# Performance work log

Hardware: AMD Instinct MI355X
Metric: run time of the kernel (lower is better)

Reference implementation:

```python
import jax, jax.numpy as jnp
import numpy as np

NEG_BIG = -1e9

def setup_inputs() -> dict:
    key = jax.random.key(0)
    kq, kk, kv, kwq, kwk, kwv, km = jax.random.split(key, 7)
    B, S, d = 16, 1024, 512
    Q = jax.random.normal(kq, (B, S, d), dtype=jnp.float32)
    K = jax.random.normal(kk, (B, S, d), dtype=jnp.float32)
    V = jax.random.normal(kv, (B, S, d), dtype=jnp.float32)
    # nn.Linear weights [d, d]; torch applies x @ W.T
    WQ = jax.random.normal(kwq, (d, d), dtype=jnp.float32) / np.sqrt(d)
    WK = jax.random.normal(kwk, (d, d), dtype=jnp.float32) / np.sqrt(d)
    WV = jax.random.normal(kwv, (d, d), dtype=jnp.float32) / np.sqrt(d)
    mask = jax.random.randint(km, (B, S), 0, 2, dtype=jnp.int32)
    return {"Q": Q, "K": K, "V": V, "WQ": WQ, "WK": WK, "WV": WV, "mask": mask}


def reference(Q, K, V, WQ, WK, WV, mask):
    d = Q.shape[-1]
    q = jnp.einsum('bsd,ed->bse', Q, WQ)
    k = jnp.einsum('bsd,ed->bse', K, WK)
    v = jnp.einsum('bsd,ed->bse', V, WV)
    scores = jnp.einsum('bqd,bkd->bqk', q, k) / jnp.sqrt(jnp.float32(d))
    attn = jax.nn.softmax(scores, axis=-1)
    # Faithful to original: mask applied AFTER softmax with -1e9 fill
    m = mask[:, None, :]  # [B,1,S] broadcast over query dim
    attn = jnp.where(m == 0, jnp.float32(NEG_BIG), attn)
    out = jnp.einsum('bqk,bkd->bqd', attn, v)
    return (out, attn)
```

## Files before the change

### kernel.cpp

```cpp
#include <hip/hip_runtime.h>
#include <hip/hip_bf16.h>

typedef float f32x4 __attribute__((ext_vector_type(4)));
typedef __bf16 bf16x8 __attribute__((ext_vector_type(8)));
typedef unsigned short u16x8 __attribute__((ext_vector_type(8)));
typedef int i32x4 __attribute__((ext_vector_type(4)));

#define NEG_BIG_F (-1000000000.0f)
#define SCALE_F 0.044194173824159216f

__device__ __forceinline__ unsigned short f2bf(float f) {
  unsigned int u = __float_as_uint(f);
  u += 0x7FFFu + ((u >> 16) & 1u);
  return (unsigned short)(u >> 16);
}

__device__ __forceinline__ float bf2f(unsigned short h) {
  return __uint_as_float((unsigned int)h << 16);
}

__device__ __forceinline__ u16x8 cvt8(f32x4 a, f32x4 b) {
  u16x8 r;
  r[0] = f2bf(a[0]); r[1] = f2bf(a[1]); r[2] = f2bf(a[2]); r[3] = f2bf(a[3]);
  r[4] = f2bf(b[0]); r[5] = f2bf(b[1]); r[6] = f2bf(b[2]); r[7] = f2bf(b[3]);
  return r;
}

__device__ __forceinline__ void gload16(const void* g, char* l) {
  __builtin_amdgcn_global_load_lds(
      (const __attribute__((address_space(1))) unsigned int*)g,
      (__attribute__((address_space(3))) unsigned int*)l, 16, 0, 0);
}

__global__ __launch_bounds__(256) void cvtW(
    const float* __restrict__ w0, const float* __restrict__ w1,
    const float* __restrict__ w2, unsigned short* __restrict__ out)
{
  const float* src = blockIdx.z == 0 ? w0 : (blockIdx.z == 1 ? w1 : w2);
  unsigned short* dst = out + (size_t)blockIdx.z * 262144;
  const int i = (blockIdx.x * 256 + threadIdx.x) * 8;
  f32x4 a = *(const f32x4*)(src + i);
  f32x4 b = *(const f32x4*)(src + i + 4);
  *(u16x8*)&dst[i] = cvt8(a, b);
}

__global__ __launch_bounds__(512, 2) void projqk(
    const float* __restrict__ Q, const float* __restrict__ Kx,
    const unsigned short* __restrict__ wb,
    unsigned short* __restrict__ qb, unsigned short* __restrict__ kb)
{
  __shared__ __align__(16) unsigned short As[2][256][32];
  __shared__ __align__(16) unsigned short Bs[2][256][32];

  const int tid = threadIdx.x, z = blockIdx.z;
  const float* X = z ? Kx : Q;
  const unsigned short* W = wb + (size_t)z * 262144;
  unsigned short* Y = z ? kb : qb;
  const int m0 = blockIdx.x * 256, n0 = blockIdx.y * 256;
  const int lane = tid & 63, wave = tid >> 6;
  const int wr = (wave >> 2) * 128, wc = (wave & 3) * 64;
  const int fr = lane & 15, fq = lane >> 4;

  f32x4 acc[8][4] = {};

  int arow_s[2], aswz_s[2];
  const float* gAs[2];
  #pragma unroll
  for (int i = 0; i < 2; i++) {
    const int c = tid + 512 * i;
    arow_s[i] = c >> 2;
    aswz_s[i] = ((c & 3) ^ ((arow_s[i] >> 1) & 3)) * 8;
    gAs[i] = X + (size_t)(m0 + arow_s[i]) * 512 + (c & 3) * 8;
  }
  const unsigned short* gB[2]; char* lB[2];
  #pragma unroll
  for (int i = 0; i < 2; i++) {
    const int c = tid + 512 * i, row = c >> 2, slot = c & 3;
    gB[i] = W + (size_t)(n0 + row) * 512 + (slot ^ ((row >> 1) & 3)) * 8;
    lB[i] = (char*)&Bs[0][0][0] + c * 16;
  }

  f32x4 pa[2][2];
  #pragma unroll
  for (int i = 0; i < 2; i++) {
    pa[i][0] = *(const f32x4*)(gAs[i]);
    pa[i][1] = *(const f32x4*)(gAs[i] + 4);
  }
  #pragma unroll
  for (int i = 0; i < 2; i++) gload16(gB[i], lB[i]);
  #pragma unroll
  for (int i = 0; i < 2; i++)
    *(u16x8*)&As[0][arow_s[i]][aswz_s[i]] = cvt8(pa[i][0], pa[i][1]);

  int cur = 0;
  for (int kt = 0; kt < 512; kt += 32) {
    const int nb = cur ^ 1;
    if (kt < 480) {
      #pragma unroll
      for (int i = 0; i < 2; i++) {
        pa[i][0] = *(const f32x4*)(gAs[i] + kt + 32);
        pa[i][1] = *(const f32x4*)(gAs[i] + kt + 36);
      }
      #pragma unroll
      for (int i = 0; i < 2; i++) gload16(gB[i] + kt + 32, lB[i] + nb * 16384);
      asm volatile("s_waitcnt vmcnt(6) lgkmcnt(0)" ::: "memory");
    } else {
      asm volatile("s_waitcnt vmcnt(0) lgkmcnt(0)" ::: "memory");
    }
    __builtin_amdgcn_sched_barrier(0);
    __builtin_amdgcn_s_barrier();

    bf16x8 bv[4];
    #pragma unroll
    for (int nf = 0; nf < 4; nf++) {
      const int br = wc + nf * 16 + fr;
      bv[nf] = *(const bf16x8*)&Bs[cur][br][(fq ^ ((br >> 1) & 3)) * 8];
    }
    #pragma unroll
    for (int mf = 0; mf < 8; mf++) {
      const int ar = wr + mf * 16 + fr;
      bf16x8 av = *(const bf16x8*)&As[cur][ar][(fq ^ ((ar >> 1) & 3)) * 8];
      #pragma unroll
      for (int nf = 0; nf < 4; nf++)
        acc[mf][nf] = __builtin_amdgcn_mfma_f32_16x16x32_bf16(av, bv[nf], acc[mf][nf], 0, 0, 0);
    }

    if (kt < 480) {
      #pragma unroll
      for (int i = 0; i < 2; i++)
        *(u16x8*)&As[nb][arow_s[i]][aswz_s[i]] = cvt8(pa[i][0], pa[i][1]);
    }
    __builtin_amdgcn_s_barrier();
    cur = nb;
  }

  #pragma unroll
  for (int mf = 0; mf < 8; mf++)
    #pragma unroll
    for (int nf = 0; nf < 4; nf++)
      #pragma unroll
      for (int rr = 0; rr < 4; rr++) {
        const int m = m0 + wr + mf * 16 + fq * 4 + rr;
        const int n = n0 + wc + nf * 16 + fr;
        Y[(size_t)m * 512 + n] = f2bf(acc[mf][nf][rr]);
      }
}

__global__ __launch_bounds__(512, 2) void projv(
    const float* __restrict__ V, const unsigned short* __restrict__ wv,
    unsigned short* __restrict__ vt)
{
  __shared__ __align__(16) unsigned short As[2][128][32];
  __shared__ __align__(16) unsigned short Bs[2][256][32];

  const int tid = threadIdx.x;
  const int m0 = blockIdx.x * 128, n0 = blockIdx.y * 256, b = blockIdx.z;
  const int lane = tid & 63, wave = tid >> 6;
  const int wr = (wave >> 2) * 64, wc = (wave & 3) * 64;
  const int fr = lane & 15, fq = lane >> 4;

  f32x4 acc[4][4] = {};

  const int ar_s = tid >> 2, aslot = tid & 3;
  const unsigned short* gA = wv + (size_t)(m0 + ar_s) * 512 + (aslot ^ ((ar_s >> 1) & 3)) * 8;
  char* lA = (char*)&As[0][0][0] + tid * 16;

  int brow_s[2], bswz_s[2];
  const float* gBs[2];
  #pragma unroll
  for (int i = 0; i < 2; i++) {
    const int c = tid + 512 * i;
    brow_s[i] = c >> 2;
    bswz_s[i] = ((c & 3) ^ ((brow_s[i] >> 1) & 3)) * 8;
    gBs[i] = V + ((size_t)b * 1024 + n0 + brow_s[i]) * 512 + (c & 3) * 8;
  }

  f32x4 pb[2][2];
  #pragma unroll
  for (int i = 0; i < 2; i++) {
    pb[i][0] = *(const f32x4*)(gBs[i]);
    pb[i][1] = *(const f32x4*)(gBs[i] + 4);
  }
  gload16(gA, lA);
  #pragma unroll
  for (int i = 0; i < 2; i++)
    *(u16x8*)&Bs[0][brow_s[i]][bswz_s[i]] = cvt8(pb[i][0], pb[i][1]);

  int cur = 0;
  for (int kt = 0; kt < 512; kt += 32) {
    const int nb = cur ^ 1;
    if (kt < 480) {
      #pragma unroll
      for (int i = 0; i < 2; i++) {
        pb[i][0] = *(const f32x4*)(gBs[i] + kt + 32);
        pb[i][1] = *(const f32x4*)(gBs[i] + kt + 36);
      }
      gload16(gA + kt + 32, lA + nb * 8192);
      asm volatile("s_waitcnt vmcnt(5) lgkmcnt(0)" ::: "memory");
    } else {
      asm volatile("s_waitcnt vmcnt(0) lgkmcnt(0)" ::: "memory");
    }
    __builtin_amdgcn_sched_barrier(0);
    __builtin_amdgcn_s_barrier();

    bf16x8 av[4], bv[4];
    #pragma unroll
    for (int mf = 0; mf < 4; mf++) {
      const int ar = wr + mf * 16 + fr;
      av[mf] = *(const bf16x8*)&As[cur][ar][(fq ^ ((ar >> 1) & 3)) * 8];
    }
    #pragma unroll
    for (int nf = 0; nf < 4; nf++) {
      const int br = wc + nf * 16 + fr;
      bv[nf] = *(const bf16x8*)&Bs[cur][br][(fq ^ ((br >> 1) & 3)) * 8];
    }
    #pragma unroll
    for (int mf = 0; mf < 4; mf++)
      #pragma unroll
      for (int nf = 0; nf < 4; nf++)
        acc[mf][nf] = __builtin_amdgcn_mfma_f32_16x16x32_bf16(av[mf], bv[nf], acc[mf][nf], 0, 0, 0);

    if (kt < 480) {
      #pragma unroll
      for (int i = 0; i < 2; i++)
        *(u16x8*)&Bs[nb][brow_s[i]][bswz_s[i]] = cvt8(pb[i][0], pb[i][1]);
    }
    __builtin_amdgcn_s_barrier();
    cur = nb;
  }

  #pragma unroll
  for (int mf = 0; mf < 4; mf++)
    #pragma unroll
    for (int nf = 0; nf < 4; nf++)
      #pragma unroll
      for (int rr = 0; rr < 4; rr++) {
        const int e = m0 + wr + mf * 16 + fq * 4 + rr;
        const int s = n0 + wc + nf * 16 + fr;
        vt[((size_t)b * 512 + e) * 1024 + s] = f2bf(acc[mf][nf][rr]);
      }
}

__global__ __launch_bounds__(512, 2) void score256(
    const unsigned short* __restrict__ qb, const unsigned short* __restrict__ kb,
    const int* __restrict__ mask,
    unsigned short* __restrict__ P, float* __restrict__ partial)
{
  __shared__ __align__(16) unsigned short As[2][256][32];
  __shared__ __align__(16) unsigned short Bs[2][256][32];

  const int tid = threadIdx.x, bz = blockIdx.z;
  const int m0 = blockIdx.x * 256, n0 = blockIdx.y * 256;
  const int lane = tid & 63, wave = tid >> 6;
  const int wr = (wave >> 2) * 128, wc = (wave & 3) * 64;
  const int fr = lane & 15, fq = lane >> 4;

  f32x4 acc[8][4] = {};

  const unsigned short* gA[2]; char* lA[2];
  const unsigned short* gB[2]; char* lB[2];
  #pragma unroll
  for (int i = 0; i < 2; i++) {
    const int c = tid + 512 * i, row = c >> 2, slot = c & 3;
    const int sw = (slot ^ ((row >> 1) & 3)) * 8;
    gA[i] = qb + ((size_t)bz * 1024 + m0 + row) * 512 + sw;
    gB[i] = kb + ((size_t)bz * 1024 + n0 + row) * 512 + sw;
    lA[i] = (char*)&As[0][0][0] + c * 16;
    lB[i] = (char*)&Bs[0][0][0] + c * 16;
  }

  #pragma unroll
  for (int i = 0; i < 2; i++) { gload16(gA[i], lA[i]); gload16(gB[i], lB[i]); }

  int cur = 0;
  for (int kt = 0; kt < 512; kt += 32) {
    const int nb = cur ^ 1;
    if (kt < 480) {
      #pragma unroll
      for (int i = 0; i < 2; i++) {
        gload16(gA[i] + kt + 32, lA[i] + nb * 16384);
        gload16(gB[i] + kt + 32, lB[i] + nb * 16384);
      }
      asm volatile("s_waitcnt vmcnt(4) lgkmcnt(0)" ::: "memory");
    } else {
      asm volatile("s_waitcnt vmcnt(0) lgkmcnt(0)" ::: "memory");
    }
    __builtin_amdgcn_sched_barrier(0);
    __builtin_amdgcn_s_barrier();

    bf16x8 bv[4];
    #pragma unroll
    for (int nf = 0; nf < 4; nf++) {
      const int br = wc + nf * 16 + fr;
      bv[nf] = *(const bf16x8*)&Bs[cur][br][(fq ^ ((br >> 1) & 3)) * 8];
    }
    #pragma unroll
    for (int mf = 0; mf < 8; mf++) {
      const int ar = wr + mf * 16 + fr;
      bf16x8 av = *(const bf16x8*)&As[cur][ar][(fq ^ ((ar >> 1) & 3)) * 8];
      #pragma unroll
      for (int nf = 0; nf < 4; nf++)
        acc[mf][nf] = __builtin_amdgcn_mfma_f32_16x16x32_bf16(av, bv[nf], acc[mf][nf], 0, 0, 0);
    }
    __builtin_amdgcn_s_barrier();
    cur = nb;
  }

  int mcol[4];
  #pragma unroll
  for (int nf = 0; nf < 4; nf++)
    mcol[nf] = mask[bz * 1024 + n0 + wc + nf * 16 + fr];

  unsigned short* Pb = P + ((size_t)bz << 20);
  const int slot = blockIdx.y * 4 + (wave & 3);
  #pragma unroll
  for (int mf = 0; mf < 8; mf++) {
    #pragma unroll
    for (int rr = 0; rr < 4; rr++) {
      const int m = m0 + wr + mf * 16 + fq * 4 + rr;
      float e = 0.f;
      #pragma unroll
      for (int nf = 0; nf < 4; nf++) {
        const float ev = __expf(acc[mf][nf][rr] * SCALE_F);
        e += ev;
        Pb[(size_t)m * 1024 + n0 + wc + nf * 16 + fr] =
            mcol[nf] ? f2bf(ev) : (unsigned short)0;
      }
      e += __shfl_xor(e, 1); e += __shfl_xor(e, 2);
      e += __shfl_xor(e, 4); e += __shfl_xor(e, 8);
      if (fr == 0)
        partial[(size_t)slot * 16384 + bz * 1024 + m] = e;
    }
  }
}

__global__ __launch_bounds__(256) void rs_inv(
    const float* __restrict__ partial, float* __restrict__ inv)
{
  const int i = blockIdx.x * 256 + threadIdx.x;
  float s = 0.f;
  #pragma unroll
  for (int p = 0; p < 16; p++) s += partial[(size_t)p * 16384 + i];
  inv[i] = 1.0f / s;
}

__global__ __launch_bounds__(256) void mvsum_k(
    const unsigned short* __restrict__ vt, const int* __restrict__ mask,
    float* __restrict__ mvsum)
{
  const int row = blockIdx.x * 4 + (threadIdx.x >> 6);
  const int b = row >> 9;
  const int lane = threadIdx.x & 63;
  const unsigned short* vr = vt + (size_t)row * 1024 + lane * 16;
  const int* mr = mask + b * 1024 + lane * 16;
  u16x8 v0 = *(const u16x8*)(vr);
  u16x8 v1 = *(const u16x8*)(vr + 8);
  float s = 0.f;
  #pragma unroll
  for (int j = 0; j < 8; j++) {
    if (!mr[j])     s += bf2f(v0[j]);
    if (!mr[8 + j]) s += bf2f(v1[j]);
  }
  #pragma unroll
  for (int o = 32; o > 0; o >>= 1) s += __shfl_xor(s, o);
  if (lane == 0) mvsum[row] = s;
}

__global__ __launch_bounds__(256) void attn_write(
    const unsigned short* __restrict__ P, const float* __restrict__ inv,
    const int* __restrict__ mask, float* __restrict__ attn)
{
  const size_t base = ((size_t)blockIdx.x * 256 + threadIdx.x) * 8;
  const int row = (int)(base >> 10);
  const int b = row >> 10;
  const int k0 = (int)(base & 1023);
  const u16x8 p8 = *(const u16x8*)(P + base);
  const float iv = inv[row];
  const int* mr = mask + b * 1024 + k0;
  const i32x4 ma = *(const i32x4*)(mr);
  const i32x4 mb = *(const i32x4*)(mr + 4);
  f32x4 o0, o1;
  o0[0] = ma[0] ? bf2f(p8[0]) * iv : NEG_BIG_F;
  o0[1] = ma[1] ? bf2f(p8[1]) * iv : NEG_BIG_F;
  o0[2] = ma[2] ? bf2f(p8[2]) * iv : NEG_BIG_F;
  o0[3] = ma[3] ? bf2f(p8[3]) * iv : NEG_BIG_F;
  o1[0] = mb[0] ? bf2f(p8[4]) * iv : NEG_BIG_F;
  o1[1] = mb[1] ? bf2f(p8[5]) * iv : NEG_BIG_F;
  o1[2] = mb[2] ? bf2f(p8[6]) * iv : NEG_BIG_F;
  o1[3] = mb[3] ? bf2f(p8[7]) * iv : NEG_BIG_F;
  *(f32x4*)(attn + base) = o0;
  *(f32x4*)(attn + base + 4) = o1;
}

__global__ __launch_bounds__(512) void pv_gemm(
    const unsigned short* __restrict__ P, const unsigned short* __restrict__ vt,
    const float* __restrict__ inv, const float* __restrict__ mvsum,
    float* __restrict__ out)
{
  __shared__ __align__(16) unsigned short As[2][64][32];
  __shared__ __align__(16) unsigned short Bs[2][512][32];

  const int tid = threadIdx.x;
  const int bz = blockIdx.z, m0 = blockIdx.x * 64;
  const int lane = tid & 63, wave = tid >> 6;
  const int n0 = wave * 64;
  const int fr = lane & 15, fq = lane >> 4;

  f32x4 acc[4][4] = {};

  const unsigned short* gA = nullptr; char* lA = nullptr;
  if (tid < 256) {
    const int row = tid >> 2, slot = tid & 3;
    gA = P + ((size_t)bz << 20) + (size_t)(m0 + row) * 1024 + (slot ^ ((row >> 1) & 3)) * 8;
    lA = (char*)&As[0][0][0] + tid * 16;
  }
  const unsigned short* gB[4]; char* lB[4];
  #pragma unroll
  for (int i = 0; i < 4; i++) {
    const int c = tid + 512 * i, row = c >> 2, slot = c & 3;
    gB[i] = vt + ((size_t)bz * 512 + row) * 1024 + (slot ^ ((row >> 1) & 3)) * 8;
    lB[i] = (char*)&Bs[0][0][0] + c * 16;
  }

  if (tid < 256) gload16(gA, lA);
  #pragma unroll
  for (int i = 0; i < 4; i++) gload16(gB[i], lB[i]);

  int cur = 0;
  for (int t = 0; t < 32; t++) {
    const int nb = cur ^ 1;
    const int kt = t * 32;
    if (t < 31) {
      if (tid < 256) gload16(gA + kt + 32, lA + nb * 4096);
      #pragma unroll
      for (int i = 0; i < 4; i++) gload16(gB[i] + kt + 32, lB[i] + nb * 32768);
      if (wave < 4) asm volatile("s_waitcnt vmcnt(5) lgkmcnt(0)" ::: "memory");
      else          asm volatile("s_waitcnt vmcnt(4) lgkmcnt(0)" ::: "memory");
    } else {
      asm volatile("s_waitcnt vmcnt(0) lgkmcnt(0)" ::: "memory");
    }
    __builtin_amdgcn_sched_barrier(0);
    __builtin_amdgcn_s_barrier();

    bf16x8 af[4], bv[4];
    #pragma unroll
    for (int mf = 0; mf < 4; mf++) {
      const int ar = mf * 16 + fr;
      af[mf] = *(const bf16x8*)&As[cur][ar][(fq ^ ((ar >> 1) & 3)) * 8];
    }
    #pragma unroll
    for (int nf = 0; nf < 4; nf++) {
      const int br = n0 + nf * 16 + fr;
      bv[nf] = *(const bf16x8*)&Bs[cur][br][(fq ^ ((br >> 1) & 3)) * 8];
    }
    #pragma unroll
    for (int mf = 0; mf < 4; mf++)
      #pragma unroll
      for (int nf = 0; nf < 4; nf++)
        acc[mf][nf] = __builtin_amdgcn_mfma_f32_16x16x32_bf16(af[mf], bv[nf], acc[mf][nf], 0, 0, 0);
    __builtin_amdgcn_s_barrier();
    cur = nb;
  }

  float mvv[4];
  #pragma unroll
  for (int nf = 0; nf < 4; nf++)
    mvv[nf] = mvsum[bz * 512 + n0 + nf * 16 + fr];
  #pragma unroll
  for (int mf = 0; mf < 4; mf++)
    #pragma unroll
    for (int rr = 0; rr < 4; rr++) {
      const int m = m0 + mf * 16 + fq * 4 + rr;
      const float iv = inv[bz * 1024 + m];
      #pragma unroll
      for (int nf = 0; nf < 4; nf++)
        out[((size_t)bz * 1024 + m) * 512 + n0 + nf * 16 + fr] =
            iv * acc[mf][nf][rr] + NEG_BIG_F * mvv[nf];
    }
}

extern "C" void kernel_launch(void* const* d_in, const int* in_sizes, int n_in,
                              void* d_out, int out_size, void* d_ws, size_t ws_size,
                              hipStream_t stream)
{
  const float* Q  = (const float*)d_in[0];
  const float* Kx = (const float*)d_in[1];
  const float* V  = (const float*)d_in[2];
  const float* WQ = (const float*)d_in[3];
  const float* WK = (const float*)d_in[4];
  const float* WV = (const float*)d_in[5];
  const int* mask = (const int*)d_in[6];

  const int B = 16, S = 1024, D = 512;
  float* out_f  = (float*)d_out;
  float* attn_f = out_f + (size_t)B * S * D;
  unsigned short* Pbuf = (unsigned short*)d_out;

  unsigned short* qb = (unsigned short*)d_ws;
  unsigned short* kb = qb + (size_t)B * S * D;
  unsigned short* vt = kb + (size_t)B * S * D;
  unsigned short* wb = vt + (size_t)B * S * D;
  float* partial = (float*)(wb + 786432);
  float* inv = partial + 262144;
  float* mvsum = inv + 16384;

  cvtW<<<dim3(128, 1, 3), 256, 0, stream>>>(WQ, WK, WV, wb);
  projqk<<<dim3(64, 2, 2), 512, 0, stream>>>(Q, Kx, wb, qb, kb);
  projv<<<dim3(4, 4, 16), 512, 0, stream>>>(V, wb + 524288, vt);
  score256<<<dim3(4, 4, 16), 512, 0, stream>>>(qb, kb, mask, Pbuf, partial);
  rs_inv<<<dim3(64), 256, 0, stream>>>(partial, inv);
  mvsum_k<<<dim3(2048), 256, 0, stream>>>(vt, mask, mvsum);
  attn_write<<<dim3(8192), 256, 0, stream>>>(Pbuf, inv, mask, attn_f);
  pv_gemm<<<dim3(16, 1, 16), 512, 0, stream>>>(Pbuf, vt, inv, mvsum, out_f);
}
```

Before: 166.2 us.

## Merge projection kernels and fold row-sum inverse into consumers

```diff
diff --git a/kernel.cpp b/kernel.cpp
--- a/kernel.cpp
+++ b/kernel.cpp
@@ -44,201 +44,203 @@
   *(u16x8*)&dst[i] = cvt8(a, b);
 }
 
-__global__ __launch_bounds__(512, 2) void projqk(
+__global__ __launch_bounds__(512, 2) void proj_all(
     const float* __restrict__ Q, const float* __restrict__ Kx,
-    const unsigned short* __restrict__ wb,
-    unsigned short* __restrict__ qb, unsigned short* __restrict__ kb)
-{
-  __shared__ __align__(16) unsigned short As[2][256][32];
-  __shared__ __align__(16) unsigned short Bs[2][256][32];
-
-  const int tid = threadIdx.x, z = blockIdx.z;
-  const float* X = z ? Kx : Q;
-  const unsigned short* W = wb + (size_t)z * 262144;
-  unsigned short* Y = z ? kb : qb;
-  const int m0 = blockIdx.x * 256, n0 = blockIdx.y * 256;
-  const int lane = tid & 63, wave = tid >> 6;
-  const int wr = (wave >> 2) * 128, wc = (wave & 3) * 64;
-  const int fr = lane & 15, fq = lane >> 4;
-
-  f32x4 acc[8][4] = {};
-
-  int arow_s[2], aswz_s[2];
-  const float* gAs[2];
-  #pragma unroll
-  for (int i = 0; i < 2; i++) {
-    const int c = tid + 512 * i;
-    arow_s[i] = c >> 2;
-    aswz_s[i] = ((c & 3) ^ ((arow_s[i] >> 1) & 3)) * 8;
-    gAs[i] = X + (size_t)(m0 + arow_s[i]) * 512 + (c & 3) * 8;
-  }
-  const unsigned short* gB[2]; char* lB[2];
-  #pragma unroll
-  for (int i = 0; i < 2; i++) {
-    const int c = tid + 512 * i, row = c >> 2, slot = c & 3;
-    gB[i] = W + (size_t)(n0 + row) * 512 + (slot ^ ((row >> 1) & 3)) * 8;
-    lB[i] = (char*)&Bs[0][0][0] + c * 16;
-  }
-
-  f32x4 pa[2][2];
-  #pragma unroll
-  for (int i = 0; i < 2; i++) {
-    pa[i][0] = *(const f32x4*)(gAs[i]);
-    pa[i][1] = *(const f32x4*)(gAs[i] + 4);
-  }
-  #pragma unroll
-  for (int i = 0; i < 2; i++) gload16(gB[i], lB[i]);
-  #pragma unroll
-  for (int i = 0; i < 2; i++)
-    *(u16x8*)&As[0][arow_s[i]][aswz_s[i]] = cvt8(pa[i][0], pa[i][1]);
-
-  int cur = 0;
-  for (int kt = 0; kt < 512; kt += 32) {
-    const int nb = cur ^ 1;
-    if (kt < 480) {
-      #pragma unroll
-      for (int i = 0; i < 2; i++) {
-        pa[i][0] = *(const f32x4*)(gAs[i] + kt + 32);
-        pa[i][1] = *(const f32x4*)(gAs[i] + kt + 36);
-      }
-      #pragma unroll
-      for (int i = 0; i < 2; i++) gload16(gB[i] + kt + 32, lB[i] + nb * 16384);
-      asm volatile("s_waitcnt vmcnt(6) lgkmcnt(0)" ::: "memory");
-    } else {
-      asm volatile("s_waitcnt vmcnt(0) lgkmcnt(0)" ::: "memory");
-    }
-    __builtin_amdgcn_sched_barrier(0);
-    __builtin_amdgcn_s_barrier();
-
-    bf16x8 bv[4];
-    #pragma unroll
-    for (int nf = 0; nf < 4; nf++) {
-      const int br = wc + nf * 16 + fr;
-      bv[nf] = *(const bf16x8*)&Bs[cur][br][(fq ^ ((br >> 1) & 3)) * 8];
-    }
-    #pragma unroll
-    for (int mf = 0; mf < 8; mf++) {
-      const int ar = wr + mf * 16 + fr;
-      bf16x8 av = *(const bf16x8*)&As[cur][ar][(fq ^ ((ar >> 1) & 3)) * 8];
-      #pragma unroll
-      for (int nf = 0; nf < 4; nf++)
-        acc[mf][nf] = __builtin_amdgcn_mfma_f32_16x16x32_bf16(av, bv[nf], acc[mf][nf], 0, 0, 0);
-    }
-
-    if (kt < 480) {
-      #pragma unroll
-      for (int i = 0; i < 2; i++)
-        *(u16x8*)&As[nb][arow_s[i]][aswz_s[i]] = cvt8(pa[i][0], pa[i][1]);
-    }
-    __builtin_amdgcn_s_barrier();
-    cur = nb;
-  }
-
-  #pragma unroll
-  for (int mf = 0; mf < 8; mf++)
-    #pragma unroll
-    for (int nf = 0; nf < 4; nf++)
-      #pragma unroll
-      for (int rr = 0; rr < 4; rr++) {
-        const int m = m0 + wr + mf * 16 + fq * 4 + rr;
-        const int n = n0 + wc + nf * 16 + fr;
-        Y[(size_t)m * 512 + n] = f2bf(acc[mf][nf][rr]);
-      }
-}
-
-__global__ __launch_bounds__(512, 2) void projv(
-    const float* __restrict__ V, const unsigned short* __restrict__ wv,
+    const float* __restrict__ V, const unsigned short* __restrict__ wb,
+    unsigned short* __restrict__ qb, unsigned short* __restrict__ kb,
     unsigned short* __restrict__ vt)
 {
-  __shared__ __align__(16) unsigned short As[2][128][32];
-  __shared__ __align__(16) unsigned short Bs[2][256][32];
-
+  __shared__ __align__(16) unsigned short lds[32768];
+
+  const int bid = blockIdx.x;
   const int tid = threadIdx.x;
-  const int m0 = blockIdx.x * 128, n0 = blockIdx.y * 256, b = blockIdx.z;
   const int lane = tid & 63, wave = tid >> 6;
-  const int wr = (wave >> 2) * 64, wc = (wave & 3) * 64;
   const int fr = lane & 15, fq = lane >> 4;
 
-  f32x4 acc[4][4] = {};
-
-  const int ar_s = tid >> 2, aslot = tid & 3;
-  const unsigned short* gA = wv + (size_t)(m0 + ar_s) * 512 + (aslot ^ ((ar_s >> 1) & 3)) * 8;
-  char* lA = (char*)&As[0][0][0] + tid * 16;
-
-  int brow_s[2], bswz_s[2];
-  const float* gBs[2];
-  #pragma unroll
-  for (int i = 0; i < 2; i++) {
-    const int c = tid + 512 * i;
-    brow_s[i] = c >> 2;
-    bswz_s[i] = ((c & 3) ^ ((brow_s[i] >> 1) & 3)) * 8;
-    gBs[i] = V + ((size_t)b * 1024 + n0 + brow_s[i]) * 512 + (c & 3) * 8;
-  }
-
-  f32x4 pb[2][2];
-  #pragma unroll
-  for (int i = 0; i < 2; i++) {
-    pb[i][0] = *(const f32x4*)(gBs[i]);
-    pb[i][1] = *(const f32x4*)(gBs[i] + 4);
-  }
-  gload16(gA, lA);
-  #pragma unroll
-  for (int i = 0; i < 2; i++)
-    *(u16x8*)&Bs[0][brow_s[i]][bswz_s[i]] = cvt8(pb[i][0], pb[i][1]);
-
-  int cur = 0;
-  for (int kt = 0; kt < 512; kt += 32) {
-    const int nb = cur ^ 1;
-    if (kt < 480) {
-      #pragma unroll
-      for (int i = 0; i < 2; i++) {
-        pb[i][0] = *(const f32x4*)(gBs[i] + kt + 32);
-        pb[i][1] = *(const f32x4*)(gBs[i] + kt + 36);
-      }
-      gload16(gA + kt + 32, lA + nb * 8192);
-      asm volatile("s_waitcnt vmcnt(5) lgkmcnt(0)" ::: "memory");
-    } else {
-      asm volatile("s_waitcnt vmcnt(0) lgkmcnt(0)" ::: "memory");
-    }
-    __builtin_amdgcn_sched_barrier(0);
-    __builtin_amdgcn_s_barrier();
-
-    bf16x8 av[4], bv[4];
-    #pragma unroll
-    for (int mf = 0; mf < 4; mf++) {
-      const int ar = wr + mf * 16 + fr;
-      av[mf] = *(const bf16x8*)&As[cur][ar][(fq ^ ((ar >> 1) & 3)) * 8];
-    }
-    #pragma unroll
-    for (int nf = 0; nf < 4; nf++) {
-      const int br = wc + nf * 16 + fr;
-      bv[nf] = *(const bf16x8*)&Bs[cur][br][(fq ^ ((br >> 1) & 3)) * 8];
-    }
+  if (bid < 256) {
+    const int z = bid >> 7, rem = bid & 127;
+    const float* X = z ? Kx : Q;
+    const unsigned short* W = wb + (size_t)z * 262144;
+    unsigned short* Y = z ? kb : qb;
+    const int m0 = (rem & 63) * 256, n0 = (rem >> 6) * 256;
+    const int wr = (wave >> 2) * 128, wc = (wave & 3) * 64;
+
+    unsigned short (*As)[256][32] = (unsigned short (*)[256][32])lds;
+    unsigned short (*Bs)[256][32] = (unsigned short (*)[256][32])(lds + 16384);
+
+    f32x4 acc[8][4] = {};
+
+    int arow_s[2], aswz_s[2];
+    const float* gAs[2];
+    #pragma unroll
+    for (int i = 0; i < 2; i++) {
+      const int c = tid + 512 * i;
+      arow_s[i] = c >> 2;
+      aswz_s[i] = ((c & 3) ^ ((arow_s[i] >> 1) & 3)) * 8;
+      gAs[i] = X + (size_t)(m0 + arow_s[i]) * 512 + (c & 3) * 8;
+    }
+    const unsigned short* gB[2]; char* lB[2];
+    #pragma unroll
+    for (int i = 0; i < 2; i++) {
+      const int c = tid + 512 * i, row = c >> 2, slot = c & 3;
+      gB[i] = W + (size_t)(n0 + row) * 512 + (slot ^ ((row >> 1) & 3)) * 8;
+      lB[i] = (char*)(lds + 16384) + c * 16;
+    }
+
+    f32x4 pa[2][2];
+    #pragma unroll
+    for (int i = 0; i < 2; i++) {
+      pa[i][0] = *(const f32x4*)(gAs[i]);
+      pa[i][1] = *(const f32x4*)(gAs[i] + 4);
+    }
+    #pragma unroll
+    for (int i = 0; i < 2; i++) gload16(gB[i], lB[i]);
+    #pragma unroll
+    for (int i = 0; i < 2; i++)
+      *(u16x8*)&As[0][arow_s[i]][aswz_s[i]] = cvt8(pa[i][0], pa[i][1]);
+
+    int cur = 0;
+    for (int kt = 0; kt < 512; kt += 32) {
+      const int nb = cur ^ 1;
+      if (kt < 480) {
+        #pragma unroll
+        for (int i = 0; i < 2; i++) {
+          pa[i][0] = *(const f32x4*)(gAs[i] + kt + 32);
+          pa[i][1] = *(const f32x4*)(gAs[i] + kt + 36);
+        }
+        #pragma unroll
+        for (int i = 0; i < 2; i++) gload16(gB[i] + kt + 32, lB[i] + nb * 16384);
+        asm volatile("s_waitcnt vmcnt(6) lgkmcnt(0)" ::: "memory");
+      } else {
+        asm volatile("s_waitcnt vmcnt(0) lgkmcnt(0)" ::: "memory");
+      }
+      __builtin_amdgcn_sched_barrier(0);
+      __builtin_amdgcn_s_barrier();
+
+      bf16x8 bv[4];
+      #pragma unroll
+      for (int nf = 0; nf < 4; nf++) {
+        const int br = wc + nf * 16 + fr;
+        bv[nf] = *(const bf16x8*)&Bs[cur][br][(fq ^ ((br >> 1) & 3)) * 8];
+      }
+      #pragma unroll
+      for (int mf = 0; mf < 8; mf++) {
+        const int ar = wr + mf * 16 + fr;
+        bf16x8 av = *(const bf16x8*)&As[cur][ar][(fq ^ ((ar >> 1) & 3)) * 8];
+        #pragma unroll
+        for (int nf = 0; nf < 4; nf++)
+          acc[mf][nf] = __builtin_amdgcn_mfma_f32_16x16x32_bf16(av, bv[nf], acc[mf][nf], 0, 0, 0);
+      }
+
+      if (kt < 480) {
+        #pragma unroll
+        for (int i = 0; i < 2; i++)
+          *(u16x8*)&As[nb][arow_s[i]][aswz_s[i]] = cvt8(pa[i][0], pa[i][1]);
+      }
+      __builtin_amdgcn_s_barrier();
+      cur = nb;
+    }
+
+    #pragma unroll
+    for (int mf = 0; mf < 8; mf++)
+      #pragma unroll
+      for (int nf = 0; nf < 4; nf++)
+        #pragma unroll
+        for (int rr = 0; rr < 4; rr++) {
+          const int m = m0 + wr + mf * 16 + fq * 4 + rr;
+          const int n = n0 + wc + nf * 16 + fr;
+          Y[(size_t)m * 512 + n] = f2bf(acc[mf][nf][rr]);
+        }
+  } else {
+    const int c0 = bid - 256;
+    const int m0 = (c0 & 3) * 128, n0 = ((c0 >> 2) & 3) * 256, b = c0 >> 4;
+    const int wr = (wave >> 2) * 64, wc = (wave & 3) * 64;
+    const unsigned short* wv = wb + 524288;
+
+    unsigned short (*As)[128][32] = (unsigned short (*)[128][32])lds;
+    unsigned short (*Bs)[256][32] = (unsigned short (*)[256][32])(lds + 8192);
+
+    f32x4 acc[4][4] = {};
+
+    const int ar_s = tid >> 2, aslot = tid & 3;
+    const unsigned short* gA = wv + (size_t)(m0 + ar_s) * 512 + (aslot ^ ((ar_s >> 1) & 3)) * 8;
+    char* lA = (char*)lds + tid * 16;
+
+    int brow_s[2], bswz_s[2];
+    const float* gBs[2];
+    #pragma unroll
+    for (int i = 0; i < 2; i++) {
+      const int c = tid + 512 * i;
+      brow_s[i] = c >> 2;
+      bswz_s[i] = ((c & 3) ^ ((brow_s[i] >> 1) & 3)) * 8;
+      gBs[i] = V + ((size_t)b * 1024 + n0 + brow_s[i]) * 512 + (c & 3) * 8;
+    }
+
+    f32x4 pb[2][2];
+    #pragma unroll
+    for (int i = 0; i < 2; i++) {
+      pb[i][0] = *(const f32x4*)(gBs[i]);
+      pb[i][1] = *(const f32x4*)(gBs[i] + 4);
+    }
+    gload16(gA, lA);
+    #pragma unroll
+    for (int i = 0; i < 2; i++)
+      *(u16x8*)&Bs[0][brow_s[i]][bswz_s[i]] = cvt8(pb[i][0], pb[i][1]);
+
+    int cur = 0;
+    for (int kt = 0; kt < 512; kt += 32) {
+      const int nb = cur ^ 1;
+      if (kt < 480) {
+        #pragma unroll
+        for (int i = 0; i < 2; i++) {
+          pb[i][0] = *(const f32x4*)(gBs[i] + kt + 32);
+          pb[i][1] = *(const f32x4*)(gBs[i] + kt + 36);
+        }
+        gload16(gA + kt + 32, lA + nb * 8192);
+        asm volatile("s_waitcnt vmcnt(5) lgkmcnt(0)" ::: "memory");
+      } else {
+        asm volatile("s_waitcnt vmcnt(0) lgkmcnt(0)" ::: "memory");
+      }
+      __builtin_amdgcn_sched_barrier(0);
+      __builtin_amdgcn_s_barrier();
+
+      bf16x8 av[4], bv[4];
+      #pragma unroll
+      for (int mf = 0; mf < 4; mf++) {
+        const int ar = wr + mf * 16 + fr;
+        av[mf] = *(const bf16x8*)&As[cur][ar][(fq ^ ((ar >> 1) & 3)) * 8];
+      }
+      #pragma unroll
+      for (int nf = 0; nf < 4; nf++) {
+        const int br = wc + nf * 16 + fr;
+        bv[nf] = *(const bf16x8*)&Bs[cur][br][(fq ^ ((br >> 1) & 3)) * 8];
+      }
+      #pragma unroll
+      for (int mf = 0; mf < 4; mf++)
+        #pragma unroll
+        for (int nf = 0; nf < 4; nf++)
+          acc[mf][nf] = __builtin_amdgcn_mfma_f32_16x16x32_bf16(av[mf], bv[nf], acc[mf][nf], 0, 0, 0);
+
+      if (kt < 480) {
+        #pragma unroll
+        for (int i = 0; i < 2; i++)
+          *(u16x8*)&Bs[nb][brow_s[i]][bswz_s[i]] = cvt8(pb[i][0], pb[i][1]);
+      }
+      __builtin_amdgcn_s_barrier();
+      cur = nb;
+    }
+
     #pragma unroll
     for (int mf = 0; mf < 4; mf++)
       #pragma unroll
       for (int nf = 0; nf < 4; nf++)
-        acc[mf][nf] = __builtin_amdgcn_mfma_f32_16x16x32_bf16(av[mf], bv[nf], acc[mf][nf], 0, 0, 0);
-
-    if (kt < 480) {
-      #pragma unroll
-      for (int i = 0; i < 2; i++)
-        *(u16x8*)&Bs[nb][brow_s[i]][bswz_s[i]] = cvt8(pb[i][0], pb[i][1]);
-    }
-    __builtin_amdgcn_s_barrier();
-    cur = nb;
-  }
-
-  #pragma unroll
-  for (int mf = 0; mf < 4; mf++)
-    #pragma unroll
-    for (int nf = 0; nf < 4; nf++)
-      #pragma unroll
-      for (int rr = 0; rr < 4; rr++) {
-        const int e = m0 + wr + mf * 16 + fq * 4 + rr;
-        const int s = n0 + wc + nf * 16 + fr;
-        vt[((size_t)b * 512 + e) * 1024 + s] = f2bf(acc[mf][nf][rr]);
-      }
+        #pragma unroll
+        for (int rr = 0; rr < 4; rr++) {
+          const int e = m0 + wr + mf * 16 + fq * 4 + rr;
+          const int s = n0 + wc + nf * 16 + fr;
+          vt[((size_t)b * 512 + e) * 1024 + s] = f2bf(acc[mf][nf][rr]);
+        }
+  }
 }
 
 __global__ __launch_bounds__(512, 2) void score256(
@@ -334,71 +336,71 @@
   }
 }
 
-__global__ __launch_bounds__(256) void rs_inv(
-    const float* __restrict__ partial, float* __restrict__ inv)
+__global__ __launch_bounds__(256) void mv_attn(
+    const unsigned short* __restrict__ vt, const unsigned short* __restrict__ P,
+    const float* __restrict__ partial, const int* __restrict__ mask,
+    float* __restrict__ mvsum, float* __restrict__ attn)
 {
-  const int i = blockIdx.x * 256 + threadIdx.x;
-  float s = 0.f;
-  #pragma unroll
-  for (int p = 0; p < 16; p++) s += partial[(size_t)p * 16384 + i];
-  inv[i] = 1.0f / s;
-}
-
-__global__ __launch_bounds__(256) void mvsum_k(
-    const unsigned short* __restrict__ vt, const int* __restrict__ mask,
-    float* __restrict__ mvsum)
-{
-  const int row = blockIdx.x * 4 + (threadIdx.x >> 6);
-  const int b = row >> 9;
-  const int lane = threadIdx.x & 63;
-  const unsigned short* vr = vt + (size_t)row * 1024 + lane * 16;
-  const int* mr = mask + b * 1024 + lane * 16;
-  u16x8 v0 = *(const u16x8*)(vr);
-  u16x8 v1 = *(const u16x8*)(vr + 8);
-  float s = 0.f;
-  #pragma unroll
-  for (int j = 0; j < 8; j++) {
-    if (!mr[j])     s += bf2f(v0[j]);
-    if (!mr[8 + j]) s += bf2f(v1[j]);
-  }
-  #pragma unroll
-  for (int o = 32; o > 0; o >>= 1) s += __shfl_xor(s, o);
-  if (lane == 0) mvsum[row] = s;
-}
-
-__global__ __launch_bounds__(256) void attn_write(
-    const unsigned short* __restrict__ P, const float* __restrict__ inv,
-    const int* __restrict__ mask, float* __restrict__ attn)
-{
-  const size_t base = ((size_t)blockIdx.x * 256 + threadIdx.x) * 8;
-  const int row = (int)(base >> 10);
-  const int b = row >> 10;
-  const int k0 = (int)(base & 1023);
-  const u16x8 p8 = *(const u16x8*)(P + base);
-  const float iv = inv[row];
-  const int* mr = mask + b * 1024 + k0;
-  const i32x4 ma = *(const i32x4*)(mr);
-  const i32x4 mb = *(const i32x4*)(mr + 4);
-  f32x4 o0, o1;
-  o0[0] = ma[0] ? bf2f(p8[0]) * iv : NEG_BIG_F;
-  o0[1] = ma[1] ? bf2f(p8[1]) * iv : NEG_BIG_F;
-  o0[2] = ma[2] ? bf2f(p8[2]) * iv : NEG_BIG_F;
-  o0[3] = ma[3] ? bf2f(p8[3]) * iv : NEG_BIG_F;
-  o1[0] = mb[0] ? bf2f(p8[4]) * iv : NEG_BIG_F;
-  o1[1] = mb[1] ? bf2f(p8[5]) * iv : NEG_BIG_F;
-  o1[2] = mb[2] ? bf2f(p8[6]) * iv : NEG_BIG_F;
-  o1[3] = mb[3] ? bf2f(p8[7]) * iv : NEG_BIG_F;
-  *(f32x4*)(attn + base) = o0;
-  *(f32x4*)(attn + base + 4) = o1;
+  const int bid = blockIdx.x;
+  const int tid = threadIdx.x;
+  if (bid < 2048) {
+    const int row = bid * 4 + (tid >> 6);
+    const int b = row >> 9;
+    const int lane = tid & 63;
+    const unsigned short* vr = vt + (size_t)row * 1024 + lane * 16;
+    const int* mr = mask + b * 1024 + lane * 16;
+    u16x8 v0 = *(const u16x8*)(vr);
+    u16x8 v1 = *(const u16x8*)(vr + 8);
+    float s = 0.f;
+    #pragma unroll
+    for (int j = 0; j < 8; j++) {
+      if (!mr[j])     s += bf2f(v0[j]);
+      if (!mr[8 + j]) s += bf2f(v1[j]);
+    }
+    #pragma unroll
+    for (int o = 32; o > 0; o >>= 1) s += __shfl_xor(s, o);
+    if (lane == 0) mvsum[row] = s;
+  } else {
+    const int ab = bid - 2048;
+    __shared__ float s_inv[2];
+    const int row0 = ab * 2;
+    if (tid < 2) {
+      float s = 0.f;
+      #pragma unroll
+      for (int p = 0; p < 16; p++) s += partial[(size_t)p * 16384 + row0 + tid];
+      s_inv[tid] = 1.0f / s;
+    }
+    __syncthreads();
+    const size_t base = (size_t)ab * 2048 + tid * 8;
+    const int b = (int)(base >> 20);
+    const int k0 = (int)(base & 1023);
+    const u16x8 p8 = *(const u16x8*)(P + base);
+    const float iv = s_inv[tid >> 7];
+    const int* mr = mask + b * 1024 + k0;
+    const i32x4 ma = *(const i32x4*)(mr);
+    const i32x4 mb = *(const i32x4*)(mr + 4);
+    f32x4 o0, o1;
+    o0[0] = ma[0] ? bf2f(p8[0]) * iv : NEG_BIG_F;
+    o0[1] = ma[1] ? bf2f(p8[1]) * iv : NEG_BIG_F;
+    o0[2] = ma[2] ? bf2f(p8[2]) * iv : NEG_BIG_F;
+    o0[3] = ma[3] ? bf2f(p8[3]) * iv : NEG_BIG_F;
+    o1[0] = mb[0] ? bf2f(p8[4]) * iv : NEG_BIG_F;
+    o1[1] = mb[1] ? bf2f(p8[5]) * iv : NEG_BIG_F;
+    o1[2] = mb[2] ? bf2f(p8[6]) * iv : NEG_BIG_F;
+    o1[3] = mb[3] ? bf2f(p8[7]) * iv : NEG_BIG_F;
+    *(f32x4*)(attn + base) = o0;
+    *(f32x4*)(attn + base + 4) = o1;
+  }
 }
 
 __global__ __launch_bounds__(512) void pv_gemm(
     const unsigned short* __restrict__ P, const unsigned short* __restrict__ vt,
-    const float* __restrict__ inv, const float* __restrict__ mvsum,
+    const float* __restrict__ partial, const float* __restrict__ mvsum,
     float* __restrict__ out)
 {
   __shared__ __align__(16) unsigned short As[2][64][32];
   __shared__ __align__(16) unsigned short Bs[2][512][32];
+  __shared__ float inv_l[64];
 
   const int tid = threadIdx.x;
   const int bz = blockIdx.z, m0 = blockIdx.x * 64;
@@ -407,6 +409,13 @@
   const int fr = lane & 15, fq = lane >> 4;
 
   f32x4 acc[4][4] = {};
+
+  if (tid < 64) {
+    float s = 0.f;
+    #pragma unroll
+    for (int p = 0; p < 16; p++) s += partial[(size_t)p * 16384 + bz * 1024 + m0 + tid];
+    inv_l[tid] = 1.0f / s;
+  }
 
   const unsigned short* gA = nullptr; char* lA = nullptr;
   if (tid < 256) {
@@ -471,7 +480,7 @@
     #pragma unroll
     for (int rr = 0; rr < 4; rr++) {
       const int m = m0 + mf * 16 + fq * 4 + rr;
-      const float iv = inv[bz * 1024 + m];
+      const float iv = inv_l[mf * 16 + fq * 4 + rr];
       #pragma unroll
       for (int nf = 0; nf < 4; nf++)
         out[((size_t)bz * 1024 + m) * 512 + n0 + nf * 16 + fr] =
@@ -501,15 +510,11 @@
   unsigned short* vt = kb + (size_t)B * S * D;
   unsigned short* wb = vt + (size_t)B * S * D;
   float* partial = (float*)(wb + 786432);
-  float* inv = partial + 262144;
-  float* mvsum = inv + 16384;
+  float* mvsum = partial + 262144;
 
   cvtW<<<dim3(128, 1, 3), 256, 0, stream>>>(WQ, WK, WV, wb);
-  projqk<<<dim3(64, 2, 2), 512, 0, stream>>>(Q, Kx, wb, qb, kb);
-  projv<<<dim3(4, 4, 16), 512, 0, stream>>>(V, wb + 524288, vt);
+  proj_all<<<dim3(512), 512, 0, stream>>>(Q, Kx, V, wb, qb, kb, vt);
   score256<<<dim3(4, 4, 16), 512, 0, stream>>>(qb, kb, mask, Pbuf, partial);
-  rs_inv<<<dim3(64), 256, 0, stream>>>(partial, inv);
-  mvsum_k<<<dim3(2048), 256, 0, stream>>>(vt, mask, mvsum);
-  attn_write<<<dim3(8192), 256, 0, stream>>>(Pbuf, inv, mask, attn_f);
-  pv_gemm<<<dim3(16, 1, 16), 512, 0, stream>>>(Pbuf, vt, inv, mvsum, out_f);
-}
+  mv_attn<<<dim3(10240), 256, 0, stream>>>(vt, Pbuf, partial, mask, mvsum, attn_f);
+  pv_gemm<<<dim3(16, 1, 16), 512, 0, stream>>>(Pbuf, vt, partial, mvsum, out_f);
+}
```

After: 149.1 us. -10.2%, faster.
